# Optimization experiments

Hardware: AMD Instinct MI355X
Metric: run time of the kernel (lower is better)

Reference implementation:

```python
import jax, jax.numpy as jnp
import numpy as np

N = 20000      # nodes
E = 160000     # edges
F_IN = 64      # node_feature_dim
HID = 256      # hidden_dim (= per-head out_channels, concat=False)
HEADS = 4
OUT = 2
BN_EPS = 1e-5


def setup_inputs() -> dict:
    key = jax.random.key(0)
    ks = jax.random.split(key, 24)
    s = 0.02

    def w(k, shape):
        return jax.random.normal(k, shape, jnp.float32) * s

    return {
        "node_feature": jax.random.normal(ks[0], (N, F_IN), jnp.float32),
        "edge_index": jax.random.randint(ks[1], (2, E), 0, N, jnp.int32),
        # layer 1 (in=F_IN)
        "wq1": w(ks[2], (F_IN, HEADS * HID)), "bq1": w(ks[3], (HEADS * HID,)),
        "wk1": w(ks[4], (F_IN, HEADS * HID)), "bk1": w(ks[5], (HEADS * HID,)),
        "wv1": w(ks[6], (F_IN, HEADS * HID)), "bv1": w(ks[7], (HEADS * HID,)),
        "ws1": w(ks[8], (F_IN, HID)),        "bs1": w(ks[9], (HID,)),
        # layer 2 (in=HID)
        "wq2": w(ks[10], (HID, HEADS * HID)), "bq2": w(ks[11], (HEADS * HID,)),
        "wk2": w(ks[12], (HID, HEADS * HID)), "bk2": w(ks[13], (HEADS * HID,)),
        "wv2": w(ks[14], (HID, HEADS * HID)), "bv2": w(ks[15], (HEADS * HID,)),
        "ws2": w(ks[16], (HID, HID)),         "bs2": w(ks[17], (HID,)),
        # batch norm affine
        "bn_gamma": jnp.ones((HID,), jnp.float32) + w(ks[18], (HID,)),
        "bn_beta": w(ks[19], (HID,)),
        # final linear
        "lin_w": w(ks[20], (HID, OUT)), "lin_b": w(ks[21], (OUT,)),
    }


def _transformer_conv(x, src, dst, wq, bq, wk, bk, wv, bv, ws, bs):
    """PyG TransformerConv, heads=HEADS, concat=False (mean over heads), root_weight."""
    n = x.shape[0]
    q = (x @ wq + bq).reshape(n, HEADS, HID)   # [N,H,C]
    k = (x @ wk + bk).reshape(n, HEADS, HID)
    v = (x @ wv + bv).reshape(n, HEADS, HID)
    # per-edge attention logits: q_i . k_j / sqrt(C)   (message j->i, i = dst)
    alpha = jnp.einsum('ehc,ehc->eh', q[dst], k[src]) / jnp.sqrt(jnp.float32(HID))  # [E,H]
    # scatter-softmax over incoming edges of each target node
    m = jax.ops.segment_max(alpha, dst, num_segments=n)
    m = jnp.where(jnp.isfinite(m), m, 0.0)  # nodes with no in-edges
    ex = jnp.exp(alpha - m[dst])
    denom = jax.ops.segment_sum(ex, dst, num_segments=n)
    a = ex / (denom[dst] + 1e-16)                          # [E,H]
    out = jax.ops.segment_sum(v[src] * a[..., None], dst, num_segments=n)  # [N,H,C]
    return out.mean(axis=1) + x @ ws + bs                  # concat=False -> head mean; + skip


def reference(node_feature, edge_index,
              wq1, bq1, wk1, bk1, wv1, bv1, ws1, bs1,
              wq2, bq2, wk2, bk2, wv2, bv2, ws2, bs2,
              bn_gamma, bn_beta, lin_w, lin_b):
    src, dst = edge_index[0], edge_index[1]
    x = _transformer_conv(node_feature, src, dst, wq1, bq1, wk1, bk1, wv1, bv1, ws1, bs1)
    x = _transformer_conv(x, src, dst, wq2, bq2, wk2, bk2, wv2, bv2, ws2, bs2)
    # BatchNorm1d (training mode: batch statistics, biased variance)
    mu = x.mean(axis=0)
    var = jnp.mean(jnp.square(x - mu), axis=0)
    x = bn_gamma * (x - mu) / jnp.sqrt(var + BN_EPS) + bn_beta
    rsu_embedding = x[0:1]                     # [1, HID]
    logits = jax.nn.relu(x @ lin_w + lin_b)    # [N, OUT]
    action_prob = jax.nn.softmax(logits, axis=1)
    return (action_prob, rsu_embedding)
```

## Files before the change

kernel.cpp:

```cpp
#include <hip/hip_runtime.h>
#include <hip/hip_bf16.h>
#include <math.h>

#define DI __device__ __forceinline__

constexpr int NN   = 20000;
constexpr int NE   = 160000;
constexpr int FIN  = 64;
constexpr int HIDC = 256;
constexpr int NH   = 4;
constexpr int NOUT = 3328;
constexpr int CAPD = 128;

typedef __attribute__((ext_vector_type(8))) short short8;
typedef __attribute__((ext_vector_type(4))) float f32x4;
typedef __attribute__((ext_vector_type(2))) float f32x2;

DI float bf2f(unsigned short u) { return __uint_as_float(((unsigned)u) << 16); }

DI unsigned fp8pack4(float a, float b, float c, float d) {
  int v = __builtin_amdgcn_cvt_pk_fp8_f32(a, b, 0, false);
  v = __builtin_amdgcn_cvt_pk_fp8_f32(c, d, v, true);
  return (unsigned)v;
}

__global__ void k_prep(const float* __restrict__ x, __hip_bfloat16* __restrict__ xb,
                       const int* __restrict__ dst, int* __restrict__ deg) {
  int gid = blockIdx.x * 256 + threadIdx.x;
  if (gid < NN * FIN) xb[gid] = __float2bfloat16(x[gid]);
  if (gid < NE) atomicAdd(&deg[dst[gid]], 1);
}

__global__ void k_scan(const int* __restrict__ deg, int* __restrict__ offs,
                       int* __restrict__ cursor, int n_) {
  __shared__ int part[1024];
  int tid = threadIdx.x;
  const int CH = (n_ + 1023) >> 10;
  int base = tid * CH;
  int s = 0;
  for (int i = 0; i < CH; ++i) { int idx = base + i; if (idx < n_) s += deg[idx]; }
  part[tid] = s;
  __syncthreads();
  for (int off = 1; off < 1024; off <<= 1) {
    int v = (tid >= off) ? part[tid - off] : 0;
    __syncthreads();
    part[tid] += v;
    __syncthreads();
  }
  int run = (tid == 0) ? 0 : part[tid - 1];
  for (int i = 0; i < CH; ++i) {
    int idx = base + i;
    if (idx < n_) { offs[idx] = run; cursor[idx] = run; run += deg[idx]; }
  }
  if (tid == 1023) offs[n_] = run;
}

__global__ void k_scatter(const int* __restrict__ dst, int* __restrict__ cursor,
                          int* __restrict__ eid, int e_) {
  int e = blockIdx.x * blockDim.x + threadIdx.x;
  if (e < e_) {
    int p = atomicAdd(&cursor[dst[e]], 1);
    eid[p] = e;
  }
}

template <int K>
__global__ void k_pack(const float* __restrict__ wq, const float* __restrict__ bq,
                       const float* __restrict__ wk, const float* __restrict__ bk,
                       const float* __restrict__ wv, const float* __restrict__ bv,
                       const float* __restrict__ ws, const float* __restrict__ bs,
                       __hip_bfloat16* __restrict__ Wt, float* __restrict__ biasp) {
  int n = blockIdx.x * 128 + threadIdx.x;
  int k = blockIdx.y;
  const float* w; const float* b; int off; int M;
  if (n < 1024)      { w = wq; b = bq; off = n;        M = 1024; }
  else if (n < 2048) { w = wk; b = bk; off = n - 1024; M = 1024; }
  else if (n < 3072) { w = wv; b = bv; off = n - 2048; M = 1024; }
  else               { w = ws; b = bs; off = n - 3072; M = 256;  }
  Wt[(size_t)n * K + k] = __float2bfloat16(w[(size_t)k * M + off]);
  if (k == 0) biasp[n] = b[off];
}

template <int K>
__global__ __launch_bounds__(256) void k_gemm_reg(
    const __hip_bfloat16* __restrict__ X, const __hip_bfloat16* __restrict__ Wt,
    const float* __restrict__ biasp,
    unsigned char* __restrict__ qb, unsigned char* __restrict__ kb,
    unsigned char* __restrict__ vb, __hip_bfloat16* __restrict__ skipb,
    int nrows, int RB, int CB) {
  __shared__ char eplds[36864];
  const int tid = threadIdx.x;

  const int nwg = RB * CB;
  int bid = blockIdx.x;
  {
    int q8 = nwg >> 3, r8 = nwg & 7;
    int xcd = bid & 7, idx = bid >> 3;
    bid = (xcd < r8 ? xcd * (q8 + 1) : r8 * (q8 + 1) + (xcd - r8) * q8) + idx;
  }
  const int bm = (bid / CB) * 128;
  const int bn = (bid % CB) * 128;
  constexpr int KT = K / 32;

  const int l = tid & 63, w = tid >> 6;
  const int wr = w >> 1, wc = w & 1;
  const int lm = l & 15, lk = l >> 4;

  const __hip_bfloat16* Ap[4];
  const __hip_bfloat16* Bp[4];
#pragma unroll
  for (int m = 0; m < 4; ++m) {
    int row = bm + wr * 64 + m * 16 + lm;
    if (row >= nrows) row = nrows - 1;
    Ap[m] = X + (size_t)row * K + lk * 8;
  }
#pragma unroll
  for (int n = 0; n < 4; ++n) {
    int col = bn + wc * 64 + n * 16 + lm;
    Bp[n] = Wt + (size_t)col * K + lk * 8;
  }

  f32x4 acc[4][4] = {};
#pragma unroll 2
  for (int kt = 0; kt < KT; ++kt) {
    short8 a[4], b[4];
#pragma unroll
    for (int m = 0; m < 4; ++m) a[m] = *(const short8*)(Ap[m] + kt * 32);
#pragma unroll
    for (int n = 0; n < 4; ++n) b[n] = *(const short8*)(Bp[n] + kt * 32);
#pragma unroll
    for (int m = 0; m < 4; ++m)
#pragma unroll
      for (int n = 0; n < 4; ++n)
        acc[m][n] = __builtin_amdgcn_mfma_f32_16x16x32_bf16(a[m], b[n], acc[m][n], 0, 0, 0);
  }

  char* ep = eplds + w * 9216;
  float bia[4];
#pragma unroll
  for (int n = 0; n < 4; ++n) bia[n] = biasp[bn + wc * 64 + n * 16 + lm];
#pragma unroll
  for (int m = 0; m < 4; ++m)
#pragma unroll
    for (int n = 0; n < 4; ++n)
#pragma unroll
      for (int r = 0; r < 4; ++r) {
        int rl = m * 16 + lk * 4 + r;
        int cl = n * 16 + lm;
        *(__hip_bfloat16*)(ep + rl * 144 + cl * 2) = __float2bfloat16(acc[m][n][r] + bia[n]);
      }
  const int c8 = l & 7;
  const int r8 = l >> 3;
#pragma unroll
  for (int it = 0; it < 8; ++it) {
    int rl = it * 8 + r8;
    int grow = bm + wr * 64 + rl;
    if (grow >= nrows) continue;
    short8 t = *(const short8*)(ep + rl * 144 + c8 * 16);
    int colg = bn + wc * 64 + c8 * 8;
    if (colg < 3072) {
      float f0 = bf2f((unsigned short)t[0]), f1 = bf2f((unsigned short)t[1]);
      float f2 = bf2f((unsigned short)t[2]), f3 = bf2f((unsigned short)t[3]);
      float f4 = bf2f((unsigned short)t[4]), f5 = bf2f((unsigned short)t[5]);
      float f6 = bf2f((unsigned short)t[6]), f7 = bf2f((unsigned short)t[7]);
      uint2 d;
      d.x = fp8pack4(f0, f1, f2, f3);
      d.y = fp8pack4(f4, f5, f6, f7);
      if (colg < 1024)      *(uint2*)(qb + (size_t)grow * 1024 + colg)        = d;
      else if (colg < 2048) *(uint2*)(kb + (size_t)grow * 1024 + colg - 1024) = d;
      else                  *(uint2*)(vb + (size_t)grow * 1024 + colg - 2048) = d;
    } else {
      *(short8*)((__hip_bfloat16*)skipb + (size_t)grow * HIDC + colg - 3072) = t;
    }
  }
}

__global__ __launch_bounds__(256) void k_attn(
    const unsigned char* __restrict__ qb, const unsigned char* __restrict__ kb,
    const unsigned char* __restrict__ vb,
    const int* __restrict__ offs, const int* __restrict__ eid,
    const int* __restrict__ src, const __hip_bfloat16* __restrict__ skipb,
    __hip_bfloat16* __restrict__ outb, float* __restrict__ outf) {
  int n = blockIdx.x;
  int s0 = offs[n], s1 = offs[n + 1];
  int deg = s1 - s0;
  int tid = threadIdx.x;
  if (deg == 0) {
    if (tid < 64) {
      int c = tid * 4;
      ushort4 sv = *(const ushort4*)((const ushort*)skipb + (size_t)n * HIDC + c);
      if (outb != nullptr) *(ushort4*)((ushort*)outb + (size_t)n * HIDC + c) = sv;
      if (outf != nullptr) {
        float* xr = outf + (size_t)n * HIDC + c;
        xr[0] = bf2f(sv.x); xr[1] = bf2f(sv.y); xr[2] = bf2f(sv.z); xr[3] = bf2f(sv.w);
      }
    }
    return;
  }
  __shared__ int ses[CAPD];
  __shared__ float red[NH][HIDC];
  int h = tid >> 6, lane = tid & 63;
  int dc = deg < CAPD ? deg : CAPD;
  for (int i = tid; i < dc; i += 256) ses[i] = src[eid[s0 + i]];
  __syncthreads();

  const int hc = h * HIDC;
  int c = lane * 4;
  unsigned qu = *(const unsigned*)(qb + (size_t)n * 1024 + hc + c);
  f32x2 q01 = __builtin_amdgcn_cvt_pk_f32_fp8(qu, false);
  f32x2 q23 = __builtin_amdgcn_cvt_pk_f32_fp8(qu, true);
  float qx = q01.x, qy = q01.y, qz = q23.x, qw = q23.y;

  float denom = 0.f;
  float4 acc = make_float4(0.f, 0.f, 0.f, 0.f);
  int sc0 = ses[0];
  unsigned ku0 = *(const unsigned*)(kb + (size_t)sc0 * 1024 + hc + c);
  unsigned vu0 = *(const unsigned*)(vb + (size_t)sc0 * 1024 + hc + c);
  for (int i = 0; i < deg; ++i) {
    unsigned ku1 = 0, vu1 = 0;
    if (i + 1 < deg) {
      int s1i = (i + 1 < CAPD) ? ses[i + 1] : src[eid[s0 + i + 1]];
      ku1 = *(const unsigned*)(kb + (size_t)s1i * 1024 + hc + c);
      vu1 = *(const unsigned*)(vb + (size_t)s1i * 1024 + hc + c);
    }
    f32x2 k01 = __builtin_amdgcn_cvt_pk_f32_fp8(ku0, false);
    f32x2 k23 = __builtin_amdgcn_cvt_pk_f32_fp8(ku0, true);
    float p = qx * k01.x + qy * k01.y + qz * k23.x + qw * k23.y;
#pragma unroll
    for (int off = 32; off > 0; off >>= 1) p += __shfl_xor(p, off);
    float wgt = __expf(p * 0.0625f);
    denom += wgt;
    f32x2 v01 = __builtin_amdgcn_cvt_pk_f32_fp8(vu0, false);
    f32x2 v23 = __builtin_amdgcn_cvt_pk_f32_fp8(vu0, true);
    acc.x = fmaf(wgt, v01.x, acc.x);
    acc.y = fmaf(wgt, v01.y, acc.y);
    acc.z = fmaf(wgt, v23.x, acc.z);
    acc.w = fmaf(wgt, v23.y, acc.w);
    ku0 = ku1; vu0 = vu1;
  }
  float dinv = 1.f / (denom + 1e-16f);
  red[h][c + 0] = acc.x * dinv;
  red[h][c + 1] = acc.y * dinv;
  red[h][c + 2] = acc.z * dinv;
  red[h][c + 3] = acc.w * dinv;
  __syncthreads();
  if (tid < 64) {
    int c0 = tid * 4;
    ushort4 sv = *(const ushort4*)((const ushort*)skipb + (size_t)n * HIDC + c0);
    float sk[4] = {bf2f(sv.x), bf2f(sv.y), bf2f(sv.z), bf2f(sv.w)};
#pragma unroll
    for (int j = 0; j < 4; ++j) {
      float m = (red[0][c0 + j] + red[1][c0 + j] + red[2][c0 + j] + red[3][c0 + j]) * 0.25f;
      float val = m + sk[j];
      if (outb != nullptr) ((ushort*)outb)[(size_t)n * HIDC + c0 + j] = (ushort)(__bfloat16_as_ushort(__float2bfloat16(val)));
      if (outf != nullptr) outf[(size_t)n * HIDC + c0 + j] = val;
    }
  }
}

__global__ void k_bnstats(const float* __restrict__ x, float* __restrict__ sums,
                          float* __restrict__ sumsq, int n_) {
  int t = threadIdx.x;
  float s = 0.f, s2 = 0.f;
  for (int r = blockIdx.x; r < n_; r += gridDim.x) {
    float vv = x[(size_t)r * HIDC + t];
    s += vv; s2 += vv * vv;
  }
  atomicAdd(&sums[t], s);
  atomicAdd(&sumsq[t], s2);
}

__global__ __launch_bounds__(256) void k_final(
    const float* __restrict__ x, const float* __restrict__ sums, const float* __restrict__ sumsq,
    const float* __restrict__ gamma, const float* __restrict__ beta,
    const float* __restrict__ lw, const float* __restrict__ lb,
    float* __restrict__ out, int n_) {
  int sub = threadIdx.x >> 6, lane = threadIdx.x & 63;
  int n = blockIdx.x * 4 + sub;
  if (n >= n_) return;
  int c = lane * 4;
  float4 sm  = *(const float4*)(sums + c);
  float4 sq  = *(const float4*)(sumsq + c);
  const float inv_n = 1.f / (float)n_;
  float mu0 = sm.x * inv_n, mu1 = sm.y * inv_n, mu2 = sm.z * inv_n, mu3 = sm.w * inv_n;
  float r0 = 1.f / sqrtf(fmaxf(sq.x * inv_n - mu0 * mu0, 0.f) + 1e-5f);
  float r1 = 1.f / sqrtf(fmaxf(sq.y * inv_n - mu1 * mu1, 0.f) + 1e-5f);
  float r2 = 1.f / sqrtf(fmaxf(sq.z * inv_n - mu2 * mu2, 0.f) + 1e-5f);
  float r3 = 1.f / sqrtf(fmaxf(sq.w * inv_n - mu3 * mu3, 0.f) + 1e-5f);
  const float* xr = x + (size_t)n * HIDC;
  float4 xv = *(const float4*)(xr + c);
  float4 gv = *(const float4*)(gamma + c);
  float4 bv = *(const float4*)(beta + c);
  float y0 = gv.x * (xv.x - mu0) * r0 + bv.x;
  float y1 = gv.y * (xv.y - mu1) * r1 + bv.y;
  float y2 = gv.z * (xv.z - mu2) * r2 + bv.z;
  float y3 = gv.w * (xv.w - mu3) * r3 + bv.w;
  float4 wa = *(const float4*)(lw + (size_t)c * 2);
  float4 wb = *(const float4*)(lw + (size_t)c * 2 + 4);
  float p0 = y0 * wa.x + y1 * wa.z + y2 * wb.x + y3 * wb.z;
  float p1 = y0 * wa.y + y1 * wa.w + y2 * wb.y + y3 * wb.w;
#pragma unroll
  for (int off = 32; off > 0; off >>= 1) {
    p0 += __shfl_xor(p0, off);
    p1 += __shfl_xor(p1, off);
  }
  if (n == 0) *(float4*)(out + (size_t)NN * 2 + c) = make_float4(y0, y1, y2, y3);
  if (lane == 0) {
    float l0 = fmaxf(p0 + lb[0], 0.f);
    float l1 = fmaxf(p1 + lb[1], 0.f);
    float m = fmaxf(l0, l1);
    float e0 = expf(l0 - m), e1 = expf(l1 - m);
    float inv = 1.f / (e0 + e1);
    out[(size_t)n * 2 + 0] = e0 * inv;
    out[(size_t)n * 2 + 1] = e1 * inv;
  }
}

extern "C" void kernel_launch(void* const* d_in, const int* in_sizes, int n_in,
                              void* d_out, int out_size, void* d_ws, size_t ws_size,
                              hipStream_t stream) {
  const float* x0  = (const float*)d_in[0];
  const int*   ei  = (const int*)d_in[1];
  const float* wq1 = (const float*)d_in[2];  const float* bq1 = (const float*)d_in[3];
  const float* wk1 = (const float*)d_in[4];  const float* bk1 = (const float*)d_in[5];
  const float* wv1 = (const float*)d_in[6];  const float* bv1 = (const float*)d_in[7];
  const float* ws1 = (const float*)d_in[8];  const float* bs1 = (const float*)d_in[9];
  const float* wq2 = (const float*)d_in[10]; const float* bq2 = (const float*)d_in[11];
  const float* wk2 = (const float*)d_in[12]; const float* bk2 = (const float*)d_in[13];
  const float* wv2 = (const float*)d_in[14]; const float* bv2 = (const float*)d_in[15];
  const float* ws2 = (const float*)d_in[16]; const float* bs2 = (const float*)d_in[17];
  const float* gam = (const float*)d_in[18]; const float* bet = (const float*)d_in[19];
  const float* lw  = (const float*)d_in[20]; const float* lb  = (const float*)d_in[21];
  const int* srcv = ei;
  const int* dstv = ei + NE;

  char* p = (char*)d_ws;
  auto take = [&](size_t bytes) {
    char* r = p;
    p += (bytes + 255) & ~(size_t)255;
    return r;
  };
  unsigned char* qbuf = (unsigned char*)take((size_t)NN * 1024);
  unsigned char* kbuf = (unsigned char*)take((size_t)NN * 1024);
  unsigned char* vbuf = (unsigned char*)take((size_t)NN * 1024);
  __hip_bfloat16* skipb = (__hip_bfloat16*)take((size_t)NN * HIDC * 2);
  __hip_bfloat16* x0b = (__hip_bfloat16*)take((size_t)NN * FIN * 2);
  __hip_bfloat16* x2b = (__hip_bfloat16*)take((size_t)NN * HIDC * 2);
  __hip_bfloat16* Wt  = (__hip_bfloat16*)take((size_t)NOUT * HIDC * 2);
  float* x3    = (float*)take((size_t)NN * HIDC * 4);
  float* biasp = (float*)take((size_t)NOUT * 4);
  float* bnbuf = (float*)take(2 * HIDC * 4);
  int* deg    = (int*)take((size_t)NN * 4);
  int* offs   = (int*)take((size_t)(NN + 1) * 4);
  int* cursor = (int*)take((size_t)NN * 4);
  int* eidb   = (int*)take((size_t)NE * 4);
  if ((size_t)(p - (char*)d_ws) > ws_size) return;

  float* sums  = bnbuf;
  float* sumsq = bnbuf + HIDC;

  hipMemsetAsync(deg, 0, (size_t)NN * 4, stream);
  hipMemsetAsync(bnbuf, 0, 2 * HIDC * 4, stream);
  k_prep<<<(NN * FIN + 255) / 256, 256, 0, stream>>>(x0, x0b, dstv, deg);
  k_scan<<<1, 1024, 0, stream>>>(deg, offs, cursor, NN);
  k_scatter<<<(NE + 255) / 256, 256, 0, stream>>>(dstv, cursor, eidb, NE);

  const int RB = (NN + 127) / 128;
  const int CB = NOUT / 128;
  k_pack<FIN><<<dim3(CB, FIN), 128, 0, stream>>>(wq1, bq1, wk1, bk1, wv1, bv1, ws1, bs1, Wt, biasp);
  k_gemm_reg<FIN><<<RB * CB, 256, 0, stream>>>(x0b, Wt, biasp, qbuf, kbuf, vbuf, skipb, NN, RB, CB);
  k_attn<<<NN, 256, 0, stream>>>(qbuf, kbuf, vbuf, offs, eidb, srcv, skipb, x2b, nullptr);
  k_pack<HIDC><<<dim3(CB, HIDC), 128, 0, stream>>>(wq2, bq2, wk2, bk2, wv2, bv2, ws2, bs2, Wt, biasp);
  k_gemm_reg<HIDC><<<RB * CB, 256, 0, stream>>>(x2b, Wt, biasp, qbuf, kbuf, vbuf, skipb, NN, RB, CB);
  k_attn<<<NN, 256, 0, stream>>>(qbuf, kbuf, vbuf, offs, eidb, srcv, skipb, nullptr, x3);
  k_bnstats<<<256, 256, 0, stream>>>(x3, sums, sumsq, NN);
  k_final<<<(NN + 3) / 4, 256, 0, stream>>>(x3, sums, sumsq, gam, bet, lw, lb, (float*)d_out, NN);
}
```

Measured before the change: 434.9 us.

## Stage GEMM tiles through LDS with async loads and persistent row chunks

Replaces the register-direct GEMM with a double-buffered LDS pipeline that uses global_load_lds to prefetch the next K-slice while MFMAs run on the current one. The grid is reshaped so each workgroup loops over a chunk of row tiles for a fixed column block, which reduces the workgroup count and reuses the bias loads. The aim is to hide global load latency and improve memory coalescing. The cost is extra barriers per K step and possible load imbalance, since 157 row tiles are split into 40 chunks of 4.

```diff
diff --git a/kernel.cpp b/kernel.cpp
--- a/kernel.cpp
+++ b/kernel.cpp
@@ -17,6 +17,11 @@
 typedef __attribute__((ext_vector_type(2))) float f32x2;
 
 DI float bf2f(unsigned short u) { return __uint_as_float(((unsigned)u) << 16); }
+
+DI void gld16(const void* g, void* l) {
+  __builtin_amdgcn_global_load_lds((const __attribute__((address_space(1))) unsigned*)g,
+                                   (__attribute__((address_space(3))) unsigned*)l, 16, 0, 0);
+}
 
 DI unsigned fp8pack4(float a, float b, float c, float d) {
   int v = __builtin_amdgcn_cvt_pk_fp8_f32(a, b, 0, false);
@@ -82,96 +87,115 @@
 }
 
 template <int K>
-__global__ __launch_bounds__(256) void k_gemm_reg(
+__global__ __launch_bounds__(256) void k_gemm_ms(
     const __hip_bfloat16* __restrict__ X, const __hip_bfloat16* __restrict__ Wt,
     const float* __restrict__ biasp,
     unsigned char* __restrict__ qb, unsigned char* __restrict__ kb,
     unsigned char* __restrict__ vb, __hip_bfloat16* __restrict__ skipb,
-    int nrows, int RB, int CB) {
-  __shared__ char eplds[36864];
+    int nrows, int CB, int NCH, int TPC, int RBtot) {
+  __shared__ char lds[36864];
   const int tid = threadIdx.x;
 
-  const int nwg = RB * CB;
+  const int nwg = CB * NCH;
   int bid = blockIdx.x;
   {
     int q8 = nwg >> 3, r8 = nwg & 7;
     int xcd = bid & 7, idx = bid >> 3;
     bid = (xcd < r8 ? xcd * (q8 + 1) : r8 * (q8 + 1) + (xcd - r8) * q8) + idx;
   }
-  const int bm = (bid / CB) * 128;
   const int bn = (bid % CB) * 128;
+  const int chunk = bid / CB;
+  const int tstart = chunk * TPC;
+  const int tend = (tstart + TPC < RBtot) ? tstart + TPC : RBtot;
   constexpr int KT = K / 32;
+
+  const int srow = tid & 127;
+  const int kb0 = (tid >> 7) * 8;
+  const int br = bn + srow;
+  const __hip_bfloat16* bx = Wt + (size_t)br * K + kb0;
 
   const int l = tid & 63, w = tid >> 6;
   const int wr = w >> 1, wc = w & 1;
   const int lm = l & 15, lk = l >> 4;
-
-  const __hip_bfloat16* Ap[4];
-  const __hip_bfloat16* Bp[4];
-#pragma unroll
-  for (int m = 0; m < 4; ++m) {
-    int row = bm + wr * 64 + m * 16 + lm;
-    if (row >= nrows) row = nrows - 1;
-    Ap[m] = X + (size_t)row * K + lk * 8;
-  }
-#pragma unroll
-  for (int n = 0; n < 4; ++n) {
-    int col = bn + wc * 64 + n * 16 + lm;
-    Bp[n] = Wt + (size_t)col * K + lk * 8;
-  }
-
-  f32x4 acc[4][4] = {};
-#pragma unroll 2
-  for (int kt = 0; kt < KT; ++kt) {
-    short8 a[4], b[4];
-#pragma unroll
-    for (int m = 0; m < 4; ++m) a[m] = *(const short8*)(Ap[m] + kt * 32);
-#pragma unroll
-    for (int n = 0; n < 4; ++n) b[n] = *(const short8*)(Bp[n] + kt * 32);
+  const int aoff = (lk * 128 + wr * 64 + lm) * 16;
+  const int boff = 8192 + (lk * 128 + wc * 64 + lm) * 16;
+
+  float bia[4];
+#pragma unroll
+  for (int n = 0; n < 4; ++n) bia[n] = biasp[bn + wc * 64 + n * 16 + lm];
+
+  for (int t = tstart; t < tend; ++t) {
+    const int bm = t * 128;
+    int ar = bm + srow; if (ar >= nrows) ar = nrows - 1;
+    const __hip_bfloat16* ax = X + (size_t)ar * K + kb0;
+
+    auto STAGE = [&](int buf, int kt) {
+      char* base = lds + buf * 16384;
+      const int ko = kt * 32;
+      gld16(ax + ko,      base + tid * 16);
+      gld16(ax + ko + 16, base + 4096 + tid * 16);
+      gld16(bx + ko,      base + 8192 + tid * 16);
+      gld16(bx + ko + 16, base + 12288 + tid * 16);
+    };
+
+    f32x4 acc[4][4] = {};
+    int cur = 0;
+    STAGE(0, 0);
+    __syncthreads();
+#pragma unroll
+    for (int kt = 0; kt < KT; ++kt) {
+      if (kt + 1 < KT) STAGE(cur ^ 1, kt + 1);
+      const char* base = lds + cur * 16384;
+      short8 a[4], b[4];
+#pragma unroll
+      for (int m = 0; m < 4; ++m) a[m] = *(const short8*)(base + aoff + m * 256);
+#pragma unroll
+      for (int n = 0; n < 4; ++n) b[n] = *(const short8*)(base + boff + n * 256);
+#pragma unroll
+      for (int m = 0; m < 4; ++m)
+#pragma unroll
+        for (int n = 0; n < 4; ++n)
+          acc[m][n] = __builtin_amdgcn_mfma_f32_16x16x32_bf16(a[m], b[n], acc[m][n], 0, 0, 0);
+      __syncthreads();
+      cur ^= 1;
+    }
+
+    char* ep = lds + w * 9216;
 #pragma unroll
     for (int m = 0; m < 4; ++m)
 #pragma unroll
       for (int n = 0; n < 4; ++n)
-        acc[m][n] = __builtin_amdgcn_mfma_f32_16x16x32_bf16(a[m], b[n], acc[m][n], 0, 0, 0);
-  }
-
-  char* ep = eplds + w * 9216;
-  float bia[4];
-#pragma unroll
-  for (int n = 0; n < 4; ++n) bia[n] = biasp[bn + wc * 64 + n * 16 + lm];
-#pragma unroll
-  for (int m = 0; m < 4; ++m)
-#pragma unroll
-    for (int n = 0; n < 4; ++n)
-#pragma unroll
-      for (int r = 0; r < 4; ++r) {
-        int rl = m * 16 + lk * 4 + r;
-        int cl = n * 16 + lm;
-        *(__hip_bfloat16*)(ep + rl * 144 + cl * 2) = __float2bfloat16(acc[m][n][r] + bia[n]);
+#pragma unroll
+        for (int r = 0; r < 4; ++r) {
+          int rl = m * 16 + lk * 4 + r;
+          int cl = n * 16 + lm;
+          *(__hip_bfloat16*)(ep + rl * 144 + cl * 2) = __float2bfloat16(acc[m][n][r] + bia[n]);
+        }
+    const int c8 = l & 7;
+    const int r8 = l >> 3;
+#pragma unroll
+    for (int it = 0; it < 8; ++it) {
+      int rl = it * 8 + r8;
+      int grow = bm + wr * 64 + rl;
+      if (grow >= nrows) continue;
+      short8 tv = *(const short8*)(ep + rl * 144 + c8 * 16);
+      int colg = bn + wc * 64 + c8 * 8;
+      if (colg < 3072) {
+        float f0 = bf2f((unsigned short)tv[0]), f1 = bf2f((unsigned short)tv[1]);
+        float f2 = bf2f((unsigned short)tv[2]), f3 = bf2f((unsigned short)tv[3]);
+        float f4 = bf2f((unsigned short)tv[4]), f5 = bf2f((unsigned short)tv[5]);
+        float f6 = bf2f((unsigned short)tv[6]), f7 = bf2f((unsigned short)tv[7]);
+        uint2 d;
+        d.x = fp8pack4(f0, f1, f2, f3);
+        d.y = fp8pack4(f4, f5, f6, f7);
+        if (colg < 1024)      *(uint2*)(qb + (size_t)grow * 1024 + colg)        = d;
+        else if (colg < 2048) *(uint2*)(kb + (size_t)grow * 1024 + colg - 1024) = d;
+        else                  *(uint2*)(vb + (size_t)grow * 1024 + colg - 2048) = d;
+      } else {
+        *(short8*)((__hip_bfloat16*)skipb + (size_t)grow * HIDC + colg - 3072) = tv;
       }
-  const int c8 = l & 7;
-  const int r8 = l >> 3;
-#pragma unroll
-  for (int it = 0; it < 8; ++it) {
-    int rl = it * 8 + r8;
-    int grow = bm + wr * 64 + rl;
-    if (grow >= nrows) continue;
-    short8 t = *(const short8*)(ep + rl * 144 + c8 * 16);
-    int colg = bn + wc * 64 + c8 * 8;
-    if (colg < 3072) {
-      float f0 = bf2f((unsigned short)t[0]), f1 = bf2f((unsigned short)t[1]);
-      float f2 = bf2f((unsigned short)t[2]), f3 = bf2f((unsigned short)t[3]);
-      float f4 = bf2f((unsigned short)t[4]), f5 = bf2f((unsigned short)t[5]);
-      float f6 = bf2f((unsigned short)t[6]), f7 = bf2f((unsigned short)t[7]);
-      uint2 d;
-      d.x = fp8pack4(f0, f1, f2, f3);
-      d.y = fp8pack4(f4, f5, f6, f7);
-      if (colg < 1024)      *(uint2*)(qb + (size_t)grow * 1024 + colg)        = d;
-      else if (colg < 2048) *(uint2*)(kb + (size_t)grow * 1024 + colg - 1024) = d;
-      else                  *(uint2*)(vb + (size_t)grow * 1024 + colg - 2048) = d;
-    } else {
-      *(short8*)((__hip_bfloat16*)skipb + (size_t)grow * HIDC + colg - 3072) = t;
     }
+    __syncthreads();
   }
 }
 
@@ -365,13 +389,16 @@
   k_scan<<<1, 1024, 0, stream>>>(deg, offs, cursor, NN);
   k_scatter<<<(NE + 255) / 256, 256, 0, stream>>>(dstv, cursor, eidb, NE);
 
-  const int RB = (NN + 127) / 128;
-  const int CB = NOUT / 128;
+  const int RBt = (NN + 127) / 128;
+  const int CB  = NOUT / 128;
+  const int NCH = 40;
+  const int TPC = (RBt + NCH - 1) / NCH;
+  const int GRID = CB * NCH;
   k_pack<FIN><<<dim3(CB, FIN), 128, 0, stream>>>(wq1, bq1, wk1, bk1, wv1, bv1, ws1, bs1, Wt, biasp);
-  k_gemm_reg<FIN><<<RB * CB, 256, 0, stream>>>(x0b, Wt, biasp, qbuf, kbuf, vbuf, skipb, NN, RB, CB);
+  k_gemm_ms<FIN><<<GRID, 256, 0, stream>>>(x0b, Wt, biasp, qbuf, kbuf, vbuf, skipb, NN, CB, NCH, TPC, RBt);
   k_attn<<<NN, 256, 0, stream>>>(qbuf, kbuf, vbuf, offs, eidb, srcv, skipb, x2b, nullptr);
   k_pack<HIDC><<<dim3(CB, HIDC), 128, 0, stream>>>(wq2, bq2, wk2, bk2, wv2, bv2, ws2, bs2, Wt, biasp);
-  k_gemm_reg<HIDC><<<RB * CB, 256, 0, stream>>>(x2b, Wt, biasp, qbuf, kbuf, vbuf, skipb, NN, RB, CB);
+  k_gemm_ms<HIDC><<<GRID, 256, 0, stream>>>(x2b, Wt, biasp, qbuf, kbuf, vbuf, skipb, NN, CB, NCH, TPC, RBt);
   k_attn<<<NN, 256, 0, stream>>>(qbuf, kbuf, vbuf, offs, eidb, srcv, skipb, nullptr, x3);
   k_bnstats<<<256, 256, 0, stream>>>(x3, sums, sumsq, NN);
   k_final<<<(NN + 3) / 4, 256, 0, stream>>>(x3, sums, sumsq, gam, bet, lw, lb, (float*)d_out, NN);
```

Result: faster. 396.9 us (-8.7%).

## Rewrite QKV GEMM as persistent single-wave kernel with register-resident weights

Applied to the files above, without the earlier changes.

Replaces the 256-thread 128x128-tile GEMM with a one-wave-per-block persistent kernel. Each wave keeps a 64-column slice of the weights in registers and loops over a chunk of 64-row tiles. The A tiles are streamed into double-buffered LDS through global_load_lds, using an XOR swizzle and a manual vmcnt wait. This aims to stop reloading weights from global memory for every tile and to overlap the loads with MFMA work. In exchange it uses many more registers for K=256 (64 short8 values), which limits occupancy, and it relies on a hand-set waitcnt for correctness.

```diff
diff --git a/kernel.cpp b/kernel.cpp
--- a/kernel.cpp
+++ b/kernel.cpp
@@ -17,6 +17,11 @@
 typedef __attribute__((ext_vector_type(2))) float f32x2;
 
 DI float bf2f(unsigned short u) { return __uint_as_float(((unsigned)u) << 16); }
+
+DI void gld16(const void* g, void* l) {
+  __builtin_amdgcn_global_load_lds((const __attribute__((address_space(1))) unsigned*)g,
+                                   (__attribute__((address_space(3))) unsigned*)l, 16, 0, 0);
+}
 
 DI unsigned fp8pack4(float a, float b, float c, float d) {
   int v = __builtin_amdgcn_cvt_pk_fp8_f32(a, b, 0, false);
@@ -82,97 +87,123 @@
 }
 
 template <int K>
-__global__ __launch_bounds__(256) void k_gemm_reg(
+__global__ __launch_bounds__(64, 2) void k_gemm_pw(
     const __hip_bfloat16* __restrict__ X, const __hip_bfloat16* __restrict__ Wt,
     const float* __restrict__ biasp,
     unsigned char* __restrict__ qb, unsigned char* __restrict__ kb,
     unsigned char* __restrict__ vb, __hip_bfloat16* __restrict__ skipb,
-    int nrows, int RB, int CB) {
-  __shared__ char eplds[36864];
-  const int tid = threadIdx.x;
-
-  const int nwg = RB * CB;
-  int bid = blockIdx.x;
+    int nrows, int NCB, int NCH, int TPC, int RT) {
+  __shared__ char lds[16384 + 2304];
+  const int l = threadIdx.x;
+
+  const int nwg = NCB * NCH;
+  const int per = nwg >> 3;
+  const int w = (blockIdx.x & 7) * per + (blockIdx.x >> 3);
+  const int chunk = w / NCB;
+  const int ct = w % NCB;
+  const int bn = ct * 64;
+  const int t0 = chunk * TPC;
+  int t1 = t0 + TPC; if (t1 > RT) t1 = RT;
+  constexpr int KT = K / 64;
+  constexpr int NS = K / 32;
+
+  const int lm = l & 15, lk = l >> 4;
+
+  short8 bfr[4 * NS];
   {
-    int q8 = nwg >> 3, r8 = nwg & 7;
-    int xcd = bid & 7, idx = bid >> 3;
-    bid = (xcd < r8 ? xcd * (q8 + 1) : r8 * (q8 + 1) + (xcd - r8) * q8) + idx;
-  }
-  const int bm = (bid / CB) * 128;
-  const int bn = (bid % CB) * 128;
-  constexpr int KT = K / 32;
-
-  const int l = tid & 63, w = tid >> 6;
-  const int wr = w >> 1, wc = w & 1;
-  const int lm = l & 15, lk = l >> 4;
-
-  const __hip_bfloat16* Ap[4];
-  const __hip_bfloat16* Bp[4];
-#pragma unroll
-  for (int m = 0; m < 4; ++m) {
-    int row = bm + wr * 64 + m * 16 + lm;
-    if (row >= nrows) row = nrows - 1;
-    Ap[m] = X + (size_t)row * K + lk * 8;
-  }
-#pragma unroll
-  for (int n = 0; n < 4; ++n) {
-    int col = bn + wc * 64 + n * 16 + lm;
-    Bp[n] = Wt + (size_t)col * K + lk * 8;
-  }
-
-  f32x4 acc[4][4] = {};
-#pragma unroll 2
-  for (int kt = 0; kt < KT; ++kt) {
-    short8 a[4], b[4];
-#pragma unroll
-    for (int m = 0; m < 4; ++m) a[m] = *(const short8*)(Ap[m] + kt * 32);
-#pragma unroll
-    for (int n = 0; n < 4; ++n) b[n] = *(const short8*)(Bp[n] + kt * 32);
-#pragma unroll
-    for (int m = 0; m < 4; ++m)
+    const __hip_bfloat16* bp = Wt + (size_t)(bn + lm) * K + lk * 8;
+#pragma unroll
+    for (int n = 0; n < 4; ++n)
+#pragma unroll
+      for (int s = 0; s < NS; ++s)
+        bfr[n * NS + s] = *(const short8*)(bp + (size_t)n * 16 * K + s * 32);
+  }
+  float bia[4];
+#pragma unroll
+  for (int n = 0; n < 4; ++n) bia[n] = biasp[bn + n * 16 + lm];
+
+  unsigned char* dst8 = nullptr; int cb8 = 0;
+  if (bn < 1024)      { dst8 = qb; cb8 = bn; }
+  else if (bn < 2048) { dst8 = kb; cb8 = bn - 1024; }
+  else if (bn < 3072) { dst8 = vb; cb8 = bn - 2048; }
+
+  const int jrow = l >> 3;
+  const int cslot = (l & 7) ^ jrow;
+  auto STAGE = [&](int buf, int t, int kt) {
+    char* db = lds + buf * 8192;
+#pragma unroll
+    for (int j = 0; j < 8; ++j) {
+      int r = t * 64 + j * 8 + jrow;
+      if (r >= nrows) r = nrows - 1;
+      gld16(X + (size_t)r * K + kt * 64 + cslot * 8, db + j * 1024 + l * 16);
+    }
+  };
+
+  int buf = 0;
+  STAGE(0, t0, 0);
+  for (int t = t0; t < t1; ++t) {
+    f32x4 acc[4][4] = {};
+#pragma unroll
+    for (int kt = 0; kt < KT; ++kt) {
+      int nt = t, nk = kt + 1;
+      if (nk == KT) { nt = (t + 1 < t1) ? t + 1 : t; nk = 0; }
+      STAGE(buf ^ 1, nt, nk);
+      asm volatile("s_waitcnt vmcnt(8)" ::: "memory");
+      const char* db = lds + buf * 8192;
+#pragma unroll
+      for (int s2 = 0; s2 < 2; ++s2) {
+        short8 a[4];
+#pragma unroll
+        for (int m = 0; m < 4; ++m) {
+          int row = m * 16 + lm;
+          a[m] = *(const short8*)(db + row * 128 + (((s2 * 4 + lk) ^ (lm & 7)) * 16));
+        }
+#pragma unroll
+        for (int m = 0; m < 4; ++m)
+#pragma unroll
+          for (int n = 0; n < 4; ++n)
+            acc[m][n] = __builtin_amdgcn_mfma_f32_16x16x32_bf16(
+                a[m], bfr[n * NS + kt * 2 + s2], acc[m][n], 0, 0, 0);
+      }
+      buf ^= 1;
+    }
+
+    char* sc = lds + 16384;
+    const int tbase = t * 64;
+    const int srow = l >> 2, qc = l & 3;
+#pragma unroll
+    for (int m = 0; m < 4; ++m) {
 #pragma unroll
       for (int n = 0; n < 4; ++n)
-        acc[m][n] = __builtin_amdgcn_mfma_f32_16x16x32_bf16(a[m], b[n], acc[m][n], 0, 0, 0);
-  }
-
-  char* ep = eplds + w * 9216;
-  float bia[4];
-#pragma unroll
-  for (int n = 0; n < 4; ++n) bia[n] = biasp[bn + wc * 64 + n * 16 + lm];
-#pragma unroll
-  for (int m = 0; m < 4; ++m)
-#pragma unroll
-    for (int n = 0; n < 4; ++n)
-#pragma unroll
-      for (int r = 0; r < 4; ++r) {
-        int rl = m * 16 + lk * 4 + r;
-        int cl = n * 16 + lm;
-        *(__hip_bfloat16*)(ep + rl * 144 + cl * 2) = __float2bfloat16(acc[m][n][r] + bia[n]);
+#pragma unroll
+        for (int r = 0; r < 4; ++r)
+          *(__hip_bfloat16*)(sc + (lk * 4 + r) * 144 + (n * 16 + lm) * 2) =
+              __float2bfloat16(acc[m][n][r] + bia[n]);
+      const char* sr = sc + srow * 144 + qc * 32;
+      short8 ta = *(const short8*)(sr);
+      short8 tb = *(const short8*)(sr + 16);
+      int grow = tbase + m * 16 + srow;
+      if (grow < nrows) {
+        if (dst8 != nullptr) {
+          uint4 d;
+          d.x = fp8pack4(bf2f((unsigned short)ta[0]), bf2f((unsigned short)ta[1]),
+                         bf2f((unsigned short)ta[2]), bf2f((unsigned short)ta[3]));
+          d.y = fp8pack4(bf2f((unsigned short)ta[4]), bf2f((unsigned short)ta[5]),
+                         bf2f((unsigned short)ta[6]), bf2f((unsigned short)ta[7]));
+          d.z = fp8pack4(bf2f((unsigned short)tb[0]), bf2f((unsigned short)tb[1]),
+                         bf2f((unsigned short)tb[2]), bf2f((unsigned short)tb[3]));
+          d.w = fp8pack4(bf2f((unsigned short)tb[4]), bf2f((unsigned short)tb[5]),
+                         bf2f((unsigned short)tb[6]), bf2f((unsigned short)tb[7]));
+          *(uint4*)(dst8 + (size_t)grow * 1024 + cb8 + qc * 16) = d;
+        } else {
+          __hip_bfloat16* sp = skipb + (size_t)grow * HIDC + (bn - 3072) + qc * 16;
+          *(short8*)(sp) = ta;
+          *(short8*)(sp + 8) = tb;
+        }
       }
-  const int c8 = l & 7;
-  const int r8 = l >> 3;
-#pragma unroll
-  for (int it = 0; it < 8; ++it) {
-    int rl = it * 8 + r8;
-    int grow = bm + wr * 64 + rl;
-    if (grow >= nrows) continue;
-    short8 t = *(const short8*)(ep + rl * 144 + c8 * 16);
-    int colg = bn + wc * 64 + c8 * 8;
-    if (colg < 3072) {
-      float f0 = bf2f((unsigned short)t[0]), f1 = bf2f((unsigned short)t[1]);
-      float f2 = bf2f((unsigned short)t[2]), f3 = bf2f((unsigned short)t[3]);
-      float f4 = bf2f((unsigned short)t[4]), f5 = bf2f((unsigned short)t[5]);
-      float f6 = bf2f((unsigned short)t[6]), f7 = bf2f((unsigned short)t[7]);
-      uint2 d;
-      d.x = fp8pack4(f0, f1, f2, f3);
-      d.y = fp8pack4(f4, f5, f6, f7);
-      if (colg < 1024)      *(uint2*)(qb + (size_t)grow * 1024 + colg)        = d;
-      else if (colg < 2048) *(uint2*)(kb + (size_t)grow * 1024 + colg - 1024) = d;
-      else                  *(uint2*)(vb + (size_t)grow * 1024 + colg - 2048) = d;
-    } else {
-      *(short8*)((__hip_bfloat16*)skipb + (size_t)grow * HIDC + colg - 3072) = t;
-    }
-  }
+    }
+  }
+  asm volatile("s_waitcnt vmcnt(0)" ::: "memory");
 }
 
 __global__ __launch_bounds__(256) void k_attn(
@@ -365,13 +396,16 @@
   k_scan<<<1, 1024, 0, stream>>>(deg, offs, cursor, NN);
   k_scatter<<<(NE + 255) / 256, 256, 0, stream>>>(dstv, cursor, eidb, NE);
 
-  const int RB = (NN + 127) / 128;
-  const int CB = NOUT / 128;
-  k_pack<FIN><<<dim3(CB, FIN), 128, 0, stream>>>(wq1, bq1, wk1, bk1, wv1, bv1, ws1, bs1, Wt, biasp);
-  k_gemm_reg<FIN><<<RB * CB, 256, 0, stream>>>(x0b, Wt, biasp, qbuf, kbuf, vbuf, skipb, NN, RB, CB);
+  const int RT  = (NN + 63) / 64;
+  const int NCB = NOUT / 64;
+  const int NCH = 40;
+  const int TPC = (RT + NCH - 1) / NCH;
+  const int GRID = NCB * NCH;
+  k_pack<FIN><<<dim3(NOUT / 128, FIN), 128, 0, stream>>>(wq1, bq1, wk1, bk1, wv1, bv1, ws1, bs1, Wt, biasp);
+  k_gemm_pw<FIN><<<GRID, 64, 0, stream>>>(x0b, Wt, biasp, qbuf, kbuf, vbuf, skipb, NN, NCB, NCH, TPC, RT);
   k_attn<<<NN, 256, 0, stream>>>(qbuf, kbuf, vbuf, offs, eidb, srcv, skipb, x2b, nullptr);
-  k_pack<HIDC><<<dim3(CB, HIDC), 128, 0, stream>>>(wq2, bq2, wk2, bk2, wv2, bv2, ws2, bs2, Wt, biasp);
-  k_gemm_reg<HIDC><<<RB * CB, 256, 0, stream>>>(x2b, Wt, biasp, qbuf, kbuf, vbuf, skipb, NN, RB, CB);
+  k_pack<HIDC><<<dim3(NOUT / 128, HIDC), 128, 0, stream>>>(wq2, bq2, wk2, bk2, wv2, bv2, ws2, bs2, Wt, biasp);
+  k_gemm_pw<HIDC><<<GRID, 64, 0, stream>>>(x2b, Wt, biasp, qbuf, kbuf, vbuf, skipb, NN, NCB, NCH, TPC, RT);
   k_attn<<<NN, 256, 0, stream>>>(qbuf, kbuf, vbuf, offs, eidb, srcv, skipb, nullptr, x3);
   k_bnstats<<<256, 256, 0, stream>>>(x3, sums, sumsq, NN);
   k_final<<<(NN + 3) / 4, 256, 0, stream>>>(x3, sums, sumsq, gam, bet, lw, lb, (float*)d_out, NN);
```

After: 362.8 us. 1.2x faster.
